# Performance work log

Hardware: AMD Instinct MI355X
Metric: run time of the kernel (lower is better)

Reference implementation:

```python
import jax, jax.numpy as jnp
import numpy as np

EMBED = 1024
HEADS = 16
HEAD_DIM = EMBED // HEADS
HIDDEN = 4096
EPS = 1e-5


def setup_inputs() -> dict:
    key = jax.random.key(0)
    ks = jax.random.split(key, 12)
    s_e = 1.0 / np.sqrt(EMBED)
    s_h = 1.0 / np.sqrt(HIDDEN)
    inp = {
        'x': jax.random.normal(ks[0], (2, 2048, EMBED), jnp.float32),
        'Wq': jax.random.uniform(ks[1], (EMBED, EMBED), jnp.float32, -s_e, s_e),
        'bq': jnp.zeros((EMBED,), jnp.float32),
        'Wk': jax.random.uniform(ks[2], (EMBED, EMBED), jnp.float32, -s_e, s_e),
        'bk': jnp.zeros((EMBED,), jnp.float32),
        'Wv': jax.random.uniform(ks[3], (EMBED, EMBED), jnp.float32, -s_e, s_e),
        'bv': jnp.zeros((EMBED,), jnp.float32),
        'Wo': jax.random.uniform(ks[4], (EMBED, EMBED), jnp.float32, -s_e, s_e),
        'bo': jnp.zeros((EMBED,), jnp.float32),
        'g1': jnp.ones((EMBED,), jnp.float32),
        'b1': jnp.zeros((EMBED,), jnp.float32),
        'W1': jax.random.uniform(ks[5], (EMBED, HIDDEN), jnp.float32, -s_e, s_e),
        'bm1': jnp.zeros((HIDDEN,), jnp.float32),
        'W2': jax.random.uniform(ks[6], (HIDDEN, EMBED), jnp.float32, -s_h, s_h),
        'bm2': jnp.zeros((EMBED,), jnp.float32),
        'g2': jnp.ones((EMBED,), jnp.float32),
        'b2': jnp.zeros((EMBED,), jnp.float32),
    }
    return inp


def _layernorm(x, g, b):
    mu = jnp.mean(x, axis=-1, keepdims=True)
    var = jnp.mean(jnp.square(x - mu), axis=-1, keepdims=True)
    return (x - mu) * jax.lax.rsqrt(var + EPS) * g + b


def _attention(x, Wq, bq, Wk, bk, Wv, bv, Wo, bo):
    b, n, d = x.shape
    def split(h):  # [b,n,d] -> [b,H,n,hd]
        return h.reshape(b, n, HEADS, HEAD_DIM).transpose(0, 2, 1, 3)
    q = split(x @ Wq + bq)
    k = split(x @ Wk + bk)
    v = split(x @ Wv + bv)
    # NOTE: original multiplies by sqrt(head_dim) (bug preserved for faithfulness)
    scores = jnp.einsum('bhqd,bhkd->bhqk', q, k) * jnp.sqrt(jnp.float32(HEAD_DIM))
    causal = jnp.tril(jnp.ones((n, n), bool))
    scores = jnp.where(causal, scores, -jnp.inf)
    attn = jax.nn.softmax(scores, axis=-1)
    out = jnp.einsum('bhqk,bhkd->bhqd', attn, v)
    out = out.transpose(0, 2, 1, 3).reshape(b, n, d)
    return out @ Wo + bo


def reference(x, Wq, bq, Wk, bk, Wv, bv, Wo, bo, g1, b1, W1, bm1, W2, bm2, g2, b2):
    res1 = x
    x = _layernorm(_attention(x, Wq, bq, Wk, bk, Wv, bv, Wo, bo), g1, b1) + res1
    res2 = x
    h = jax.nn.gelu(x @ W1 + bm1, approximate=False) @ W2 + bm2
    return _layernorm(h, g2, b2) + res2
```

## Files before the change

kernel.cpp:

```cpp
#include <hip/hip_runtime.h>
#include <stdint.h>

typedef unsigned short u16;
typedef short short8 __attribute__((ext_vector_type(8)));
typedef float f32x4 __attribute__((ext_vector_type(4)));
typedef u16 u16x4 __attribute__((ext_vector_type(4)));
typedef u16 u16x8 __attribute__((ext_vector_type(8)));

#define MODE_F32  0
#define MODE_GELU 2
#define MODE_VT   4

#define QSCALE 11.5415603271f

__device__ __forceinline__ float b2f(u16 v) {
    union { uint32_t u; float f; } x; x.u = ((uint32_t)v) << 16; return x.f;
}
__device__ __forceinline__ u16 f2b(float f) {
    union { float f; uint32_t u; } x; x.f = f;
    uint32_t u = x.u;
    return (u16)((u + 0x7FFFu + ((u >> 16) & 1u)) >> 16);
}
__device__ __forceinline__ u16 f2b_trunc(float f) {
    union { float f; uint32_t u; } x; x.f = f;
    return (u16)(x.u >> 16);
}

#define ASYNC16(gp, lp)                                                        \
    __builtin_amdgcn_global_load_lds(                                          \
        (const __attribute__((address_space(1))) uint32_t*)(const void*)(gp),  \
        (__attribute__((address_space(3))) uint32_t*)(void*)(lp), 16, 0, 0)

#define MFMA16(a, b, c) __builtin_amdgcn_mfma_f32_16x16x32_bf16((a), (b), (c), 0, 0, 0)

__global__ __launch_bounds__(256) void split_f32(
    const float* __restrict__ in, u16* __restrict__ hi, u16* __restrict__ lo)
{
    const int i = (blockIdx.x * 256 + threadIdx.x) * 4;
    f32x4 v = *(const f32x4*)&in[i];
    u16x4 h, l;
    for (int k = 0; k < 4; k++) {
        h[k] = f2b(v[k]);
        l[k] = f2b(v[k] - b2f(h[k]));
    }
    *(u16x4*)&hi[i] = h;
    *(u16x4*)&lo[i] = l;
}

__global__ __launch_bounds__(256) void transpose_f32_bf16(
    const float* __restrict__ inA, u16* __restrict__ outA,
    const float* __restrict__ inB, u16* __restrict__ outB, int rows, int cols)
{
    const float* in = blockIdx.z ? inB : inA;
    u16* out = blockIdx.z ? outB : outA;
    __shared__ float t[32][33];
    const int r0 = blockIdx.y * 32, c0 = blockIdx.x * 32;
    const int tr = threadIdx.x >> 3, tc = (threadIdx.x & 7) * 4;
    f32x4 v = *(const f32x4*)&in[(size_t)(r0 + tr) * cols + c0 + tc];
    for (int i = 0; i < 4; i++) t[tr][tc + i] = v[i];
    __syncthreads();
    u16x4 ov;
    for (int i = 0; i < 4; i++) ov[i] = f2b(t[tc + i][tr]);
    *(u16x4*)&out[(size_t)(c0 + tr) * rows + r0 + tc] = ov;
}

__global__ __launch_bounds__(256) void transpose_split_f32(
    const float* __restrict__ inA, u16* __restrict__ hiA, u16* __restrict__ loA,
    const float* __restrict__ inB, u16* __restrict__ hiB, u16* __restrict__ loB,
    int rows, int cols)
{
    const float* in = blockIdx.z ? inB : inA;
    u16* hi = blockIdx.z ? hiB : hiA;
    u16* lo = blockIdx.z ? loB : loA;
    __shared__ float t[32][33];
    const int r0 = blockIdx.y * 32, c0 = blockIdx.x * 32;
    const int tr = threadIdx.x >> 3, tc = (threadIdx.x & 7) * 4;
    f32x4 v = *(const f32x4*)&in[(size_t)(r0 + tr) * cols + c0 + tc];
    for (int i = 0; i < 4; i++) t[tr][tc + i] = v[i];
    __syncthreads();
    u16x4 hv, lv;
    for (int i = 0; i < 4; i++) {
        const float f = t[tc + i][tr];
        hv[i] = f2b(f);
        lv[i] = f2b(f - b2f(hv[i]));
    }
    const size_t o = (size_t)(c0 + tr) * rows + r0 + tc;
    *(u16x4*)&hi[o] = hv;
    *(u16x4*)&lo[o] = lv;
}

__global__ __launch_bounds__(512) void gemm_qk_x3(
    const u16* __restrict__ Ahi, const u16* __restrict__ Alo,
    const u16* __restrict__ Bhi, const u16* __restrict__ Blo,
    const float* __restrict__ bq, const float* __restrict__ bk,
    u16* __restrict__ Qhi, u16* __restrict__ Qlo,
    u16* __restrict__ Khi, u16* __restrict__ Klo)
{
    const int K = 1024;
    __shared__ __align__(16) u16 SM[32768];
    u16* lAh = SM;          u16* lAl = SM + 8192;
    u16* lBh = SM + 16384;  u16* lBl = SM + 24576;

    const int tid = threadIdx.x;
    const int w = tid >> 6, lane = tid & 63;
    const int lane15 = lane & 15, q = lane >> 4;
    const int tM = blockIdx.y * 128, tN = blockIdx.x * 128;
    const int m0 = (w >> 1) * 32, n0 = (w & 1) * 64;

    f32x4 acc[2][4];
    for (int i = 0; i < 2; i++)
        for (int j = 0; j < 4; j++)
            acc[i][j] = (f32x4){0.f, 0.f, 0.f, 0.f};

    const int srow = lane >> 2, sch = lane & 3;
    const u16* Ah = Ahi + (size_t)tM * K;
    const u16* Al = Alo + (size_t)tM * K;
    const u16* Bh = Bhi + (size_t)tN * K;
    const u16* Bl = Blo + (size_t)tN * K;
    const size_t roff = (size_t)((w * 4) & 7) * 16 * K;

    #define STAGE_QK(buf_off, k0)                                              \
        for (int ii = 0; ii < 4; ii++) {                                       \
            const int id = w * 4 + ii, op = id >> 3, ch = id & 7;              \
            const u16* src = op == 0 ? Ah : op == 1 ? Al : op == 2 ? Bh : Bl;  \
            u16* dst = op == 0 ? lAh : op == 1 ? lAl : op == 2 ? lBh : lBl;    \
            ASYNC16(src + (size_t)(ch * 16 + srow) * K + (k0) + sch * 8,       \
                    dst + (buf_off) + ch * 512);                               \
        }

    STAGE_QK(0, 0)

    const int NT = K / 32;
    for (int kt = 0; kt < NT; kt++) {
        __syncthreads();
        const int cb = (kt & 1) * 4096, nb = 4096 - cb;
        if (kt + 1 < NT) {
            const int k0 = (kt + 1) * 32;
            STAGE_QK(nb, k0)
        }
        short8 afh[2], afl[2], bfh[4], bfl[4];
        for (int i = 0; i < 2; i++) {
            const int o = cb + (m0 + i * 16 + lane15) * 32 + q * 8;
            afh[i] = *(const short8*)&lAh[o];
            afl[i] = *(const short8*)&lAl[o];
        }
        for (int j = 0; j < 4; j++) {
            const int o = cb + (n0 + j * 16 + lane15) * 32 + q * 8;
            bfh[j] = *(const short8*)&lBh[o];
            bfl[j] = *(const short8*)&lBl[o];
        }
        for (int i = 0; i < 2; i++)
            for (int j = 0; j < 4; j++) {
                acc[i][j] = MFMA16(afh[i], bfh[j], acc[i][j]);
                acc[i][j] = MFMA16(afh[i], bfl[j], acc[i][j]);
                acc[i][j] = MFMA16(afl[i], bfh[j], acc[i][j]);
            }
    }

    const bool isQ = (tN < 1024);
    u16* dhi = isQ ? Qhi : Khi;
    u16* dlo = isQ ? Qlo : Klo;
    const int cN = isQ ? tN : (tN - 1024);
    const float scl = isQ ? QSCALE : 1.0f;
    u16* sC = SM;
    for (int pass = 0; pass < 2; pass++) {
        __syncthreads();
        for (int i = 0; i < 2; i++) {
            const int rl0 = m0 + i * 16 + q * 4;
            for (int j = 0; j < 4; j++) {
                const int cl = n0 + j * 16 + lane15;
                const float bv = isQ ? bq[cN + cl] : bk[cN + cl];
                for (int r = 0; r < 4; r++) {
                    const float v = (acc[i][j][r] + bv) * scl;
                    const u16 hv = f2b(v);
                    sC[(rl0 + r) * 136 + cl] = pass == 0 ? hv : f2b(v - b2f(hv));
                }
            }
        }
        __syncthreads();
        u16* dst = pass == 0 ? dhi : dlo;
        for (int t8 = 0; t8 < 4; t8++) {
            const int rl = t8 * 32 + (tid >> 4), cl = (tid & 15) * 8;
            *(u16x8*)&dst[(size_t)(tM + rl) * 1024 + cN + cl] = *(const u16x8*)&sC[rl * 136 + cl];
        }
    }
}

__global__ __launch_bounds__(512) void gemm_bt(
    const u16* __restrict__ A, const u16* __restrict__ Bt, const float* __restrict__ bias,
    int M, int N, int K, int mode,
    float* __restrict__ outF, u16* __restrict__ outB, size_t pstride)
{
    __shared__ __align__(16) u16 SM[17408];
    u16* lA = SM;
    u16* lB = SM + 8192;

    const int tid = threadIdx.x;
    const int w = tid >> 6, lane = tid & 63;
    const int lane15 = lane & 15, q = lane >> 4;
    const int tM = blockIdx.y * 128, tN = blockIdx.x * 128;
    const int m0 = (w >> 1) * 32, n0 = (w & 1) * 64;

    const int kchunk = K / gridDim.z;
    const int koff = blockIdx.z * kchunk;
    outF += (size_t)blockIdx.z * pstride;

    f32x4 acc[2][4];
    for (int i = 0; i < 2; i++)
        for (int j = 0; j < 4; j++)
            acc[i][j] = (f32x4){0.f, 0.f, 0.f, 0.f};

    const int srow = lane >> 2, sch = lane & 3;
    const u16* Abase = A + (size_t)tM * K + koff;
    const u16* Bbase = Bt + (size_t)tN * K + koff;
    #define STAGE_BT(buf_off, k0)                                              \
        for (int ii = 0; ii < 2; ii++) {                                       \
            const int id = w * 2 + ii;                                         \
            const u16* src = id < 8 ? Abase : Bbase;                           \
            u16* dst = id < 8 ? lA : lB;                                       \
            const int ch = id & 7;                                             \
            ASYNC16(src + (size_t)(ch * 16 + srow) * K + (k0) + sch * 8,       \
                    dst + (buf_off) + ch * 512);                               \
        }

    STAGE_BT(0, 0)

    const int NT = kchunk / 32;
    for (int kt = 0; kt < NT; kt++) {
        __syncthreads();
        const int cb = (kt & 1) * 4096, nb = 4096 - cb;
        if (kt + 1 < NT) {
            const int k0 = (kt + 1) * 32;
            STAGE_BT(nb, k0)
        }
        short8 af[2], bf[4];
        for (int i = 0; i < 2; i++) af[i] = *(const short8*)&lA[cb + (m0 + i * 16 + lane15) * 32 + q * 8];
        for (int j = 0; j < 4; j++) bf[j] = *(const short8*)&lB[cb + (n0 + j * 16 + lane15) * 32 + q * 8];
        for (int i = 0; i < 2; i++)
            for (int j = 0; j < 4; j++)
                acc[i][j] = MFMA16(af[i], bf[j], acc[i][j]);
    }

    if (mode == MODE_F32) {
        for (int i = 0; i < 2; i++) {
            const int rb = tM + m0 + i * 16 + q * 4;
            for (int j = 0; j < 4; j++) {
                const int col = tN + n0 + j * 16 + lane15;
                const float bv = (bias && blockIdx.z == 0) ? bias[col] : 0.f;
                for (int r = 0; r < 4; r++)
                    outF[(size_t)(rb + r) * N + col] = acc[i][j][r] + bv;
            }
        }
        return;
    }

    u16* sC = SM;
    __syncthreads();
    if (mode == MODE_GELU) {
        for (int i = 0; i < 2; i++) {
            const int rl0 = m0 + i * 16 + q * 4;
            for (int j = 0; j < 4; j++) {
                const int cl = n0 + j * 16 + lane15;
                const float bv = bias[tN + cl];
                for (int r = 0; r < 4; r++) {
                    float v = acc[i][j][r] + bv;
                    v = 0.5f * v * (1.f + erff(v * 0.70710678118f));
                    sC[(rl0 + r) * 136 + cl] = f2b(v);
                }
            }
        }
        __syncthreads();
        for (int t8 = 0; t8 < 4; t8++) {
            const int rl = t8 * 32 + (tid >> 4), cl = (tid & 15) * 8;
            *(u16x8*)&outB[(size_t)(tM + rl) * N + tN + cl] = *(const u16x8*)&sC[rl * 136 + cl];
        }
    } else {
        for (int i = 0; i < 2; i++) {
            const int rl0 = m0 + i * 16 + q * 4;
            for (int j = 0; j < 4; j++) {
                const int cl = n0 + j * 16 + lane15;
                const float bv = bias[tN + cl];
                for (int r = 0; r < 4; r++)
                    sC[cl * 136 + rl0 + r] = f2b(acc[i][j][r] + bv);
            }
        }
        __syncthreads();
        const int bb = tM >> 11, nbase = tM & 2047;
        for (int t8 = 0; t8 < 4; t8++) {
            const int cl = t8 * 32 + (tid >> 4), rl = (tid & 15) * 8;
            const int colg = tN + cl;
            u16* dst = &outB[((size_t)(bb * 16 + (colg >> 6)) * 64 + (colg & 63)) * 2048 + nbase + rl];
            *(u16x8*)dst = *(const u16x8*)&sC[cl * 136 + rl];
        }
    }
}

__global__ __launch_bounds__(256) void attn_fwd(
    const u16* __restrict__ Qhig, const u16* __restrict__ Qlog,
    const u16* __restrict__ Khig, const u16* __restrict__ Klog,
    const u16* __restrict__ Vtg, u16* __restrict__ Og)
{
    __shared__ u16 lQh[2][2048], lQl[2][2048];
    __shared__ u16 lKh[2][2][1024], lKl[2][2][1024];
    __shared__ u16 lV[2][2048];

    const int tid = threadIdx.x, w = tid >> 6, lane = tid & 63;
    const int lane15 = lane & 15, q = lane >> 4;
    const int bh = blockIdx.x & 31;
    const int u = blockIdx.x >> 5;
    const int qb = (u & 1) ? (u >> 1) : (31 - (u >> 1));
    const int b = bh >> 4, h = bh & 15;

    const size_t xoff = (size_t)b * 2048 * 1024 + h * 64;
    const u16* Qh_ = Qhig + xoff;
    const u16* Ql_ = Qlog + xoff;
    const u16* Kh_ = Khig + xoff;
    const u16* Kl_ = Klog + xoff;
    const u16* Vbh = Vtg + (size_t)bh * 64 * 2048;
    u16* Obh = Og + xoff;

    u16* lP = &lQh[0][0] + w * 640;

    const int srow = lane >> 2, sch = lane & 3;
    const float NEG = -3.0e38f;
    const int qrow0 = qb * 64;
    const int wrow0 = qrow0 + w * 16;
    const int ntiles = 2 * qb + 2;

    short8 ones;
    for (int i = 0; i < 8; i++) ones[i] = (short)0x3F80;

    for (int ii = 0; ii < 4; ii++) {
        const int id = w * 4 + ii;
        const int idq = id & 7, ks = idq >> 2, p = idq & 3;
        const size_t so = (size_t)(qrow0 + p * 16 + srow) * 1024 + ks * 32 + sch * 8;
        if (id < 8) ASYNC16(Qh_ + so, &lQh[ks][p * 512]);
        else        ASYNC16(Ql_ + so, &lQl[ks][p * 512]);
    }
    for (int ii = 0; ii < 3; ii++) {
        const int id = w * 3 + ii;
        if (id < 8) {
            const int sel = id >> 2, idk = id & 3, ks = idk >> 1, hh = idk & 1;
            const size_t so = (size_t)(hh * 16 + srow) * 1024 + ks * 32 + sch * 8;
            if (sel == 0) ASYNC16(Kh_ + so, &lKh[0][ks][hh * 512]);
            else          ASYNC16(Kl_ + so, &lKl[0][ks][hh * 512]);
        } else {
            const int p = id - 8;
            ASYNC16(Vbh + (size_t)(p * 16 + srow) * 2048 + sch * 8, &lV[0][p * 512]);
        }
    }

    f32x4 o[4];
    for (int j = 0; j < 4; j++) o[j] = (f32x4){0.f, 0.f, 0.f, 0.f};
    float mrow[4], lrow[4];
    for (int r = 0; r < 4; r++) { mrow[r] = NEG; lrow[r] = 0.f; }
    short8 aqh0 = {}, aqh1 = {}, aql0 = {}, aql1 = {};

    for (int t = 0; t < ntiles; t++) {
        __syncthreads();
        const int cur = t & 1, nxt = cur ^ 1;
        if (t == 0) {
            const int o0 = (w * 16 + lane15) * 32 + q * 8;
            aqh0 = *(const short8*)&lQh[0][o0];
            aqh1 = *(const short8*)&lQh[1][o0];
            aql0 = *(const short8*)&lQl[0][o0];
            aql1 = *(const short8*)&lQl[1][o0];
            __syncthreads();
        }
        if (t + 1 < ntiles) {
            const int kk1 = (t + 1) * 32;
            for (int ii = 0; ii < 3; ii++) {
                const int id = w * 3 + ii;
                if (id < 8) {
                    const int sel = id >> 2, idk = id & 3, ks = idk >> 1, hh = idk & 1;
                    const size_t so = (size_t)(kk1 + hh * 16 + srow) * 1024 + ks * 32 + sch * 8;
                    if (sel == 0) ASYNC16(Kh_ + so, &lKh[nxt][ks][hh * 512]);
                    else          ASYNC16(Kl_ + so, &lKl[nxt][ks][hh * 512]);
                } else {
                    const int p = id - 8;
                    ASYNC16(Vbh + (size_t)(p * 16 + srow) * 2048 + kk1 + sch * 8,
                            &lV[nxt][p * 512]);
                }
            }
        }
        const int kk0 = t * 32;
        if (kk0 > wrow0 + 15) continue;

        f32x4 s[2];
        for (int sub = 0; sub < 2; sub++) {
            const int ko = (sub * 16 + lane15) * 32 + q * 8;
            short8 bkh0 = *(const short8*)&lKh[cur][0][ko];
            short8 bkh1 = *(const short8*)&lKh[cur][1][ko];
            short8 bkl0 = *(const short8*)&lKl[cur][0][ko];
            short8 bkl1 = *(const short8*)&lKl[cur][1][ko];
            f32x4 z = (f32x4){0.f, 0.f, 0.f, 0.f};
            z = MFMA16(aqh0, bkh0, z);
            z = MFMA16(aqh1, bkh1, z);
            z = MFMA16(aqh0, bkl0, z);
            z = MFMA16(aqh1, bkl1, z);
            z = MFMA16(aql0, bkh0, z);
            z = MFMA16(aql1, bkh1, z);
            s[sub] = z;
        }
        const int rbase = wrow0 + q * 4;
        if (kk0 + 31 > wrow0) {
            for (int sub = 0; sub < 2; sub++)
                for (int r = 0; r < 4; r++) {
                    const int key = kk0 + sub * 16 + lane15;
                    if (key > rbase + r) s[sub][r] = NEG;
                }
        }
        float mx[4];
        for (int r = 0; r < 4; r++) mx[r] = fmaxf(s[0][r], s[1][r]);
        for (int d = 1; d < 16; d <<= 1)
            for (int r = 0; r < 4; r++) mx[r] = fmaxf(mx[r], __shfl_xor(mx[r], d));
        float alpha[4];
        for (int r = 0; r < 4; r++) {
            const float mnew = fmaxf(mrow[r], mx[r]);
            alpha[r] = __builtin_exp2f(mrow[r] - mnew);
            mrow[r] = mnew;
        }
        for (int sub = 0; sub < 2; sub++)
            for (int r = 0; r < 4; r++) {
                const float p = __builtin_exp2f(s[sub][r] - mrow[r]);
                lP[(q * 4 + r) * 40 + sub * 16 + lane15] = f2b_trunc(p);
            }
        short8 ap = *(const short8*)&lP[lane15 * 40 + q * 8];
        f32x4 zs = (f32x4){0.f, 0.f, 0.f, 0.f};
        zs = MFMA16(ap, ones, zs);
        for (int r = 0; r < 4; r++) lrow[r] = lrow[r] * alpha[r] + zs[r];
        for (int j = 0; j < 4; j++)
            for (int r = 0; r < 4; r++) o[j][r] *= alpha[r];
        for (int j = 0; j < 4; j++) {
            short8 bv = *(const short8*)&lV[cur][(j * 16 + lane15) * 32 + q * 8];
            o[j] = MFMA16(ap, bv, o[j]);
        }
    }
    float inv[4];
    for (int r = 0; r < 4; r++) inv[r] = 1.0f / lrow[r];
    for (int j = 0; j < 4; j++)
        for (int r = 0; r < 4; r++)
            Obh[(size_t)(qrow0 + w * 16 + q * 4 + r) * 1024 + j * 16 + lane15] =
                f2b(o[j][r] * inv[r]);
}

__global__ __launch_bounds__(256) void ln_res(
    const float* __restrict__ Xa, const float* __restrict__ Xb,
    const float* __restrict__ resF, const u16* __restrict__ resB,
    const float* __restrict__ g, const float* __restrict__ bb,
    u16* __restrict__ outB, float* __restrict__ outF)
{
    const int w = threadIdx.x >> 6, lane = threadIdx.x & 63;
    const int row = blockIdx.x * 4 + w;
    const size_t rowo = (size_t)row * 1024;
    f32x4 v[4];
    float s = 0.f, ss = 0.f;
    for (int i = 0; i < 4; i++) {
        const int c0 = (i * 64 + lane) * 4;
        v[i] = *(const f32x4*)&Xa[rowo + c0];
        if (Xb) {
            f32x4 v2 = *(const f32x4*)&Xb[rowo + c0];
            for (int k = 0; k < 4; k++) v[i][k] += v2[k];
        }
        for (int k = 0; k < 4; k++) { s += v[i][k]; ss += v[i][k] * v[i][k]; }
    }
    for (int d = 1; d < 64; d <<= 1) { s += __shfl_xor(s, d); ss += __shfl_xor(ss, d); }
    const float mu = s * (1.f / 1024.f);
    const float var = ss * (1.f / 1024.f) - mu * mu;
    const float rstd = rsqrtf(var + 1e-5f);
    for (int i = 0; i < 4; i++) {
        const int c0 = (i * 64 + lane) * 4;
        f32x4 gv = *(const f32x4*)&g[c0];
        f32x4 bv = *(const f32x4*)&bb[c0];
        f32x4 rv;
        if (resF) rv = *(const f32x4*)&resF[rowo + c0];
        else {
            u16x4 rb = *(const u16x4*)&resB[rowo + c0];
            for (int k = 0; k < 4; k++) rv[k] = b2f(rb[k]);
        }
        f32x4 ov;
        for (int k = 0; k < 4; k++)
            ov[k] = (v[i][k] - mu) * rstd * gv[k] + bv[k] + rv[k];
        if (outF) *(f32x4*)&outF[rowo + c0] = ov;
        if (outB) {
            u16x4 ob;
            for (int k = 0; k < 4; k++) ob[k] = f2b(ov[k]);
            *(u16x4*)&outB[rowo + c0] = ob;
        }
    }
}

extern "C" void kernel_launch(void* const* d_in, const int* in_sizes, int n_in,
                              void* d_out, int out_size, void* d_ws, size_t ws_size,
                              hipStream_t stream)
{
    const float* x   = (const float*)d_in[0];
    const float* Wq  = (const float*)d_in[1];  const float* bq  = (const float*)d_in[2];
    const float* Wk  = (const float*)d_in[3];  const float* bk  = (const float*)d_in[4];
    const float* Wv  = (const float*)d_in[5];  const float* bv  = (const float*)d_in[6];
    const float* Wo  = (const float*)d_in[7];  const float* bo  = (const float*)d_in[8];
    const float* g1  = (const float*)d_in[9];  const float* b1  = (const float*)d_in[10];
    const float* W1  = (const float*)d_in[11]; const float* bm1 = (const float*)d_in[12];
    const float* W2  = (const float*)d_in[13]; const float* bm2 = (const float*)d_in[14];
    const float* g2  = (const float*)d_in[15]; const float* b2  = (const float*)d_in[16];

    const size_t MB = (size_t)1 << 20;
    char* ws = (char*)d_ws;
    u16* xhi    = (u16*)(ws + 0 * MB);
    u16* xlo    = (u16*)(ws + 8 * MB);
    u16* WqkThi = (u16*)(ws + 16 * MB);
    u16* WqkTlo = (u16*)(ws + 20 * MB);
    u16* WvT    = (u16*)(ws + 24 * MB);
    u16* WoT    = (u16*)(ws + 26 * MB);
    u16* W1T    = (u16*)(ws + 32 * MB);
    u16* W2T    = (u16*)(ws + 40 * MB);
    u16* Qhi    = (u16*)(ws + 48 * MB);
    u16* Qlo    = (u16*)(ws + 56 * MB);
    u16* Khi    = (u16*)(ws + 64 * MB);
    u16* Klo    = (u16*)(ws + 72 * MB);
    u16* Vtb    = (u16*)(ws + 80 * MB);
    u16* aout   = (u16*)(ws + 16 * MB);
    float* O1   = (float*)(ws + 48 * MB);
    float* O2   = (float*)(ws + 64 * MB);
    u16* x1b    = (u16*)(ws + 80 * MB);
    u16* Hb     = (u16*)(ws + 0 * MB);
    float* H2a  = (float*)(ws + 48 * MB);
    float* H2b  = (float*)(ws + 64 * MB);

    split_f32<<<4096, 256, 0, stream>>>(x, xhi, xlo);
    transpose_split_f32<<<dim3(32, 32, 2), 256, 0, stream>>>(
        Wq, WqkThi, WqkTlo,
        Wk, WqkThi + 1024 * 1024, WqkTlo + 1024 * 1024, 1024, 1024);
    transpose_f32_bf16<<<dim3(32, 32, 2), 256, 0, stream>>>(Wv, WvT, Wo, WoT, 1024, 1024);
    transpose_f32_bf16<<<dim3(128, 32), 256, 0, stream>>>(W1, W1T, nullptr, nullptr, 1024, 4096);
    transpose_f32_bf16<<<dim3(32, 128), 256, 0, stream>>>(W2, W2T, nullptr, nullptr, 4096, 1024);

    gemm_qk_x3<<<dim3(16, 32), 512, 0, stream>>>(xhi, xlo, WqkThi, WqkTlo, bq, bk,
                                                 Qhi, Qlo, Khi, Klo);
    gemm_bt<<<dim3(8, 32), 512, 0, stream>>>(xhi, WvT, bv, 4096, 1024, 1024,
                                             MODE_VT, nullptr, Vtb, 0);

    attn_fwd<<<dim3(1024), 256, 0, stream>>>(Qhi, Qlo, Khi, Klo, Vtb, aout);

    gemm_bt<<<dim3(8, 32, 2), 512, 0, stream>>>(aout, WoT, bo, 4096, 1024, 1024,
                                                MODE_F32, O1, nullptr, (size_t)16 * MB / 4);
    ln_res<<<1024, 256, 0, stream>>>(O1, O2, x, nullptr, g1, b1, x1b, nullptr);

    gemm_bt<<<dim3(32, 32), 512, 0, stream>>>(x1b, W1T, bm1, 4096, 4096, 1024,
                                              MODE_GELU, nullptr, Hb, 0);
    gemm_bt<<<dim3(8, 32, 2), 512, 0, stream>>>(Hb, W2T, bm2, 4096, 1024, 4096,
                                                MODE_F32, H2a, nullptr, (size_t)16 * MB / 4);
    ln_res<<<1024, 256, 0, stream>>>(H2a, H2b, nullptr, x1b, g2, b2, nullptr, (float*)d_out);
}
```

Baseline: 449.6 us.

## Restructure attention: pair causal q-blocks per CTA, 64-key tiles, lazy rescale

The attention kernel now processes two complementary causal query blocks (qb and 31-qb) per workgroup, halving the grid and balancing work across CTAs. Key tiles grow from 32 to 64 rows with an XOR-swizzled shared-memory layout, and Q fragments are loaded straight from global memory instead of being staged in LDS. The causal mask is applied only on the diagonal tile, and the online-softmax rescale runs only when a row max grows beyond a threshold. The intent is fewer barriers, less per-tile overhead and fewer bank conflicts, at the cost of fewer resident blocks and a thresholded rescale that relies on the fp32 range.

```diff
diff --git a/kernel.cpp b/kernel.cpp
--- a/kernel.cpp
+++ b/kernel.cpp
@@ -300,15 +300,15 @@
     const u16* __restrict__ Khig, const u16* __restrict__ Klog,
     const u16* __restrict__ Vtg, u16* __restrict__ Og)
 {
-    __shared__ u16 lQh[2][2048], lQl[2][2048];
-    __shared__ u16 lKh[2][2][1024], lKl[2][2][1024];
-    __shared__ u16 lV[2][2048];
+    __shared__ __align__(16) u16 lKh[2][4096];
+    __shared__ __align__(16) u16 lKl[2][4096];
+    __shared__ __align__(16) u16 lV [2][4096];
+    __shared__ __align__(16) u16 lPb[4][1152];
 
     const int tid = threadIdx.x, w = tid >> 6, lane = tid & 63;
     const int lane15 = lane & 15, q = lane >> 4;
     const int bh = blockIdx.x & 31;
-    const int u = blockIdx.x >> 5;
-    const int qb = (u & 1) ? (u >> 1) : (31 - (u >> 1));
+    const int pr = blockIdx.x >> 5;
     const int b = bh >> 4, h = bh & 15;
 
     const size_t xoff = (size_t)b * 2048 * 1024 + h * 64;
@@ -319,129 +319,126 @@
     const u16* Vbh = Vtg + (size_t)bh * 64 * 2048;
     u16* Obh = Og + xoff;
 
-    u16* lP = &lQh[0][0] + w * 640;
-
-    const int srow = lane >> 2, sch = lane & 3;
+    u16* lP = lPb[w];
     const float NEG = -3.0e38f;
-    const int qrow0 = qb * 64;
-    const int wrow0 = qrow0 + w * 16;
-    const int ntiles = 2 * qb + 2;
+    const float THR = 11.5415603271f;
+
+    const int rsub = lane >> 3;
+    const int csw  = ((lane & 7) ^ rsub) * 8;
+    const int swz  = (lane15 & 7) << 3;
 
     short8 ones;
     for (int i = 0; i < 8; i++) ones[i] = (short)0x3F80;
 
-    for (int ii = 0; ii < 4; ii++) {
-        const int id = w * 4 + ii;
-        const int idq = id & 7, ks = idq >> 2, p = idq & 3;
-        const size_t so = (size_t)(qrow0 + p * 16 + srow) * 1024 + ks * 32 + sch * 8;
-        if (id < 8) ASYNC16(Qh_ + so, &lQh[ks][p * 512]);
-        else        ASYNC16(Ql_ + so, &lQl[ks][p * 512]);
-    }
-    for (int ii = 0; ii < 3; ii++) {
-        const int id = w * 3 + ii;
-        if (id < 8) {
-            const int sel = id >> 2, idk = id & 3, ks = idk >> 1, hh = idk & 1;
-            const size_t so = (size_t)(hh * 16 + srow) * 1024 + ks * 32 + sch * 8;
-            if (sel == 0) ASYNC16(Kh_ + so, &lKh[0][ks][hh * 512]);
-            else          ASYNC16(Kl_ + so, &lKl[0][ks][hh * 512]);
-        } else {
-            const int p = id - 8;
-            ASYNC16(Vbh + (size_t)(p * 16 + srow) * 2048 + sch * 8, &lV[0][p * 512]);
-        }
-    }
-
-    f32x4 o[4];
-    for (int j = 0; j < 4; j++) o[j] = (f32x4){0.f, 0.f, 0.f, 0.f};
-    float mrow[4], lrow[4];
-    for (int r = 0; r < 4; r++) { mrow[r] = NEG; lrow[r] = 0.f; }
-    short8 aqh0 = {}, aqh1 = {}, aql0 = {}, aql1 = {};
-
-    for (int t = 0; t < ntiles; t++) {
-        __syncthreads();
-        const int cur = t & 1, nxt = cur ^ 1;
-        if (t == 0) {
-            const int o0 = (w * 16 + lane15) * 32 + q * 8;
-            aqh0 = *(const short8*)&lQh[0][o0];
-            aqh1 = *(const short8*)&lQh[1][o0];
-            aql0 = *(const short8*)&lQl[0][o0];
-            aql1 = *(const short8*)&lQl[1][o0];
+#define STAGE_KV(buf, k0)                                                      \
+    for (int ii = 0; ii < 6; ii++) {                                           \
+        const int id = w * 6 + ii, sel = id >> 3, c = id & 7;                  \
+        if (sel == 0)                                                          \
+            ASYNC16(Kh_ + (size_t)((k0) + c * 8 + rsub) * 1024 + csw,          \
+                    &lKh[buf][c * 512]);                                       \
+        else if (sel == 1)                                                     \
+            ASYNC16(Kl_ + (size_t)((k0) + c * 8 + rsub) * 1024 + csw,          \
+                    &lKl[buf][c * 512]);                                       \
+        else                                                                   \
+            ASYNC16(Vbh + (size_t)(c * 8 + rsub) * 2048 + (k0) + csw,          \
+                    &lV[buf][c * 512]);                                        \
+    }
+
+    for (int ph = 0; ph < 2; ph++) {
+        const int qb = ph ? (31 - pr) : pr;
+        const int qrow0 = qb * 64;
+        const int wrow0 = qrow0 + w * 16;
+        const int ntiles = qb + 1;
+
+        const size_t qro = (size_t)(wrow0 + lane15) * 1024;
+        short8 aqh0 = *(const short8*)&Qh_[qro + q * 8];
+        short8 aqh1 = *(const short8*)&Qh_[qro + 32 + q * 8];
+        short8 aql0 = *(const short8*)&Ql_[qro + q * 8];
+        short8 aql1 = *(const short8*)&Ql_[qro + 32 + q * 8];
+
+        if (ph) __syncthreads();
+        STAGE_KV(0, 0)
+
+        f32x4 o[4];
+        for (int j = 0; j < 4; j++) o[j] = (f32x4){0.f, 0.f, 0.f, 0.f};
+        float mrow[4], lrow[4];
+        for (int r = 0; r < 4; r++) { mrow[r] = NEG; lrow[r] = 0.f; }
+
+        for (int t = 0; t < ntiles; t++) {
             __syncthreads();
-        }
-        if (t + 1 < ntiles) {
-            const int kk1 = (t + 1) * 32;
-            for (int ii = 0; ii < 3; ii++) {
-                const int id = w * 3 + ii;
-                if (id < 8) {
-                    const int sel = id >> 2, idk = id & 3, ks = idk >> 1, hh = idk & 1;
-                    const size_t so = (size_t)(kk1 + hh * 16 + srow) * 1024 + ks * 32 + sch * 8;
-                    if (sel == 0) ASYNC16(Kh_ + so, &lKh[nxt][ks][hh * 512]);
-                    else          ASYNC16(Kl_ + so, &lKl[nxt][ks][hh * 512]);
-                } else {
-                    const int p = id - 8;
-                    ASYNC16(Vbh + (size_t)(p * 16 + srow) * 2048 + kk1 + sch * 8,
-                            &lV[nxt][p * 512]);
+            const int cur = t & 1, nxt = cur ^ 1;
+            if (t + 1 < ntiles) {
+                STAGE_KV(nxt, (t + 1) * 64)
+            }
+            const int kk0 = t * 64;
+
+            f32x4 s[4];
+            for (int sub = 0; sub < 4; sub++) {
+                const int kb = (sub * 16 + lane15) * 64;
+                short8 bkh0 = *(const short8*)&lKh[cur][kb + ((q * 8) ^ swz)];
+                short8 bkh1 = *(const short8*)&lKh[cur][kb + ((32 + q * 8) ^ swz)];
+                short8 bkl0 = *(const short8*)&lKl[cur][kb + ((q * 8) ^ swz)];
+                short8 bkl1 = *(const short8*)&lKl[cur][kb + ((32 + q * 8) ^ swz)];
+                f32x4 z = (f32x4){0.f, 0.f, 0.f, 0.f};
+                z = MFMA16(aqh0, bkh0, z);
+                z = MFMA16(aqh1, bkh1, z);
+                z = MFMA16(aqh0, bkl0, z);
+                z = MFMA16(aqh1, bkl1, z);
+                z = MFMA16(aql0, bkh0, z);
+                z = MFMA16(aql1, bkh1, z);
+                s[sub] = z;
+            }
+            if (t == ntiles - 1) {
+                const int rbase = wrow0 + q * 4;
+                for (int sub = 0; sub < 4; sub++)
+                    for (int r = 0; r < 4; r++) {
+                        const int key = kk0 + sub * 16 + lane15;
+                        if (key > rbase + r) s[sub][r] = NEG;
+                    }
+            }
+            float mx[4];
+            for (int r = 0; r < 4; r++)
+                mx[r] = fmaxf(fmaxf(s[0][r], s[1][r]), fmaxf(s[2][r], s[3][r]));
+            for (int d = 1; d < 16; d <<= 1)
+                for (int r = 0; r < 4; r++) mx[r] = fmaxf(mx[r], __shfl_xor(mx[r], d));
+            bool need = false;
+            for (int r = 0; r < 4; r++) need |= (mx[r] > mrow[r] + THR);
+            if (__any(need)) {
+                for (int r = 0; r < 4; r++) {
+                    const float mnew = fmaxf(mrow[r], mx[r]);
+                    const float alpha = __builtin_exp2f(mrow[r] - mnew);
+                    mrow[r] = mnew;
+                    lrow[r] *= alpha;
+                    for (int j = 0; j < 4; j++) o[j][r] *= alpha;
                 }
             }
-        }
-        const int kk0 = t * 32;
-        if (kk0 > wrow0 + 15) continue;
-
-        f32x4 s[2];
-        for (int sub = 0; sub < 2; sub++) {
-            const int ko = (sub * 16 + lane15) * 32 + q * 8;
-            short8 bkh0 = *(const short8*)&lKh[cur][0][ko];
-            short8 bkh1 = *(const short8*)&lKh[cur][1][ko];
-            short8 bkl0 = *(const short8*)&lKl[cur][0][ko];
-            short8 bkl1 = *(const short8*)&lKl[cur][1][ko];
-            f32x4 z = (f32x4){0.f, 0.f, 0.f, 0.f};
-            z = MFMA16(aqh0, bkh0, z);
-            z = MFMA16(aqh1, bkh1, z);
-            z = MFMA16(aqh0, bkl0, z);
-            z = MFMA16(aqh1, bkl1, z);
-            z = MFMA16(aql0, bkh0, z);
-            z = MFMA16(aql1, bkh1, z);
-            s[sub] = z;
-        }
-        const int rbase = wrow0 + q * 4;
-        if (kk0 + 31 > wrow0) {
-            for (int sub = 0; sub < 2; sub++)
+            for (int sub = 0; sub < 4; sub++)
                 for (int r = 0; r < 4; r++) {
-                    const int key = kk0 + sub * 16 + lane15;
-                    if (key > rbase + r) s[sub][r] = NEG;
+                    const float p = __builtin_exp2f(s[sub][r] - mrow[r]);
+                    lP[(q * 4 + r) * 72 + sub * 16 + lane15] = f2b_trunc(p);
                 }
-        }
-        float mx[4];
-        for (int r = 0; r < 4; r++) mx[r] = fmaxf(s[0][r], s[1][r]);
-        for (int d = 1; d < 16; d <<= 1)
-            for (int r = 0; r < 4; r++) mx[r] = fmaxf(mx[r], __shfl_xor(mx[r], d));
-        float alpha[4];
-        for (int r = 0; r < 4; r++) {
-            const float mnew = fmaxf(mrow[r], mx[r]);
-            alpha[r] = __builtin_exp2f(mrow[r] - mnew);
-            mrow[r] = mnew;
-        }
-        for (int sub = 0; sub < 2; sub++)
-            for (int r = 0; r < 4; r++) {
-                const float p = __builtin_exp2f(s[sub][r] - mrow[r]);
-                lP[(q * 4 + r) * 40 + sub * 16 + lane15] = f2b_trunc(p);
-            }
-        short8 ap = *(const short8*)&lP[lane15 * 40 + q * 8];
-        f32x4 zs = (f32x4){0.f, 0.f, 0.f, 0.f};
-        zs = MFMA16(ap, ones, zs);
-        for (int r = 0; r < 4; r++) lrow[r] = lrow[r] * alpha[r] + zs[r];
+            short8 ap0 = *(const short8*)&lP[lane15 * 72 + q * 8];
+            short8 ap1 = *(const short8*)&lP[lane15 * 72 + 32 + q * 8];
+            f32x4 zs = (f32x4){0.f, 0.f, 0.f, 0.f};
+            zs = MFMA16(ap0, ones, zs);
+            zs = MFMA16(ap1, ones, zs);
+            for (int r = 0; r < 4; r++) lrow[r] += zs[r];
+            for (int j = 0; j < 4; j++) {
+                const int vb = (j * 16 + lane15) * 64;
+                short8 bv0 = *(const short8*)&lV[cur][vb + ((q * 8) ^ swz)];
+                short8 bv1 = *(const short8*)&lV[cur][vb + ((32 + q * 8) ^ swz)];
+                o[j] = MFMA16(ap0, bv0, o[j]);
+                o[j] = MFMA16(ap1, bv1, o[j]);
+            }
+        }
+        float inv[4];
+        for (int r = 0; r < 4; r++) inv[r] = 1.0f / lrow[r];
         for (int j = 0; j < 4; j++)
-            for (int r = 0; r < 4; r++) o[j][r] *= alpha[r];
-        for (int j = 0; j < 4; j++) {
-            short8 bv = *(const short8*)&lV[cur][(j * 16 + lane15) * 32 + q * 8];
-            o[j] = MFMA16(ap, bv, o[j]);
-        }
-    }
-    float inv[4];
-    for (int r = 0; r < 4; r++) inv[r] = 1.0f / lrow[r];
-    for (int j = 0; j < 4; j++)
-        for (int r = 0; r < 4; r++)
-            Obh[(size_t)(qrow0 + w * 16 + q * 4 + r) * 1024 + j * 16 + lane15] =
-                f2b(o[j][r] * inv[r]);
+            for (int r = 0; r < 4; r++)
+                Obh[(size_t)(wrow0 + q * 4 + r) * 1024 + j * 16 + lane15] =
+                    f2b(o[j][r] * inv[r]);
+    }
+#undef STAGE_KV
 }
 
 __global__ __launch_bounds__(256) void ln_res(
@@ -540,7 +537,7 @@
     gemm_bt<<<dim3(8, 32), 512, 0, stream>>>(xhi, WvT, bv, 4096, 1024, 1024,
                                              MODE_VT, nullptr, Vtb, 0);
 
-    attn_fwd<<<dim3(1024), 256, 0, stream>>>(Qhi, Qlo, Khi, Klo, Vtb, aout);
+    attn_fwd<<<dim3(512), 256, 0, stream>>>(Qhi, Qlo, Khi, Klo, Vtb, aout);
 
     gemm_bt<<<dim3(8, 32, 2), 512, 0, stream>>>(aout, WoT, bo, 4096, 1024, 1024,
                                                 MODE_F32, O1, nullptr, (size_t)16 * MB / 4);
```

New measurement: 430.9 us. 1.04x faster.
